# Optimization experiments

Measured on AMD Instinct MI355X. Metric: run time of the kernel, lower is better.

## Reference

```python
import jax, jax.numpy as jnp
import numpy as np

B, T, V, C, L, H = 4, 1024, 32000, 768, 6, 12
HD = C // H  # head size 64
EPS = 1e-5


def _ln(x, s, b):
    mu = jnp.mean(x, axis=-1, keepdims=True)
    var = jnp.var(x, axis=-1, keepdims=True)
    return (x - mu) * jax.lax.rsqrt(var + EPS) * s + b


def setup_inputs() -> dict:
    key = jax.random.key(0)
    ks = jax.random.split(key, 12)
    p = lambda k, shape: jax.random.normal(k, shape, jnp.float32) * 0.02
    return {
        "idx": jax.random.randint(ks[0], (B, T), 0, V),
        "targets": jax.random.randint(ks[1], (B, T), 0, V),
        "tok_emb": p(ks[2], (V, C)),
        "pos_emb": p(ks[3], (T, C)),
        "Wq": p(ks[4], (L, H, C, HD)),
        "Wk": p(ks[5], (L, H, C, HD)),
        "Wv": p(ks[6], (L, H, C, HD)),
        "ln1_s": jnp.ones((L, C), jnp.float32),
        "ln1_b": jnp.zeros((L, C), jnp.float32),
        "ln2_s": jnp.ones((L, C), jnp.float32),
        "ln2_b": jnp.zeros((L, C), jnp.float32),
        "W1": p(ks[7], (L, C, 4 * C)),
        "b1": jnp.zeros((L, 4 * C), jnp.float32),
        "W2": p(ks[8], (L, 4 * C, C)),
        "b2": jnp.zeros((L, C), jnp.float32),
        "lnf_s": jnp.ones((C,), jnp.float32),
        "lnf_b": jnp.zeros((C,), jnp.float32),
        "Wout": p(ks[9], (C, V)),
        "bout": jnp.zeros((V,), jnp.float32),
    }


def reference(idx, targets, tok_emb, pos_emb, Wq, Wk, Wv, ln1_s, ln1_b, ln2_s, ln2_b,
              W1, b1, W2, b2, lnf_s, lnf_b, Wout, bout):
    x = tok_emb[idx] + pos_emb[None, :T, :]  # [B,T,C]
    mask = jnp.tril(jnp.ones((T, T), bool))
    scale = HD ** -0.5
    for l in range(L):  # fixed small layer count
        xn = _ln(x, ln1_s[l], ln1_b[l])
        q = jnp.einsum('btc,hcd->bhtd', xn, Wq[l])
        k = jnp.einsum('btc,hcd->bhtd', xn, Wk[l])
        v = jnp.einsum('btc,hcd->bhtd', xn, Wv[l])
        scores = jnp.einsum('bhtd,bhsd->bhts', q, k) * scale
        scores = jnp.where(mask[None, None], scores, -jnp.inf)
        w = jax.nn.softmax(scores, axis=-1)
        att = jnp.einsum('bhts,bhsd->bhtd', w, v)
        # concat heads in order, matching torch.cat over ModuleList
        x = x + att.transpose(0, 2, 1, 3).reshape(B, T, C)
        xn2 = _ln(x, ln2_s[l], ln2_b[l])
        h = jax.nn.relu(jnp.einsum('btc,cf->btf', xn2, W1[l]) + b1[l])
        x = x + jnp.einsum('btf,fc->btc', h, W2[l]) + b2[l]
    x = _ln(x, lnf_s, lnf_b)
    logits = jnp.einsum('btc,cv->btv', x, Wout) + bout
    logits = logits.reshape(B * T, V)
    lp = jax.nn.log_softmax(logits, axis=-1)
    loss = -jnp.mean(lp[jnp.arange(B * T), targets.reshape(-1)])
    return logits, loss
```

## Files before the change

kernel.cpp:

```cpp
#include <hip/hip_runtime.h>
#include <hip/hip_bf16.h>


typedef __attribute__((ext_vector_type(8))) short          bh8;
typedef __attribute__((ext_vector_type(4))) unsigned short us4;
typedef __attribute__((ext_vector_type(4))) float          fl4;

__device__ inline unsigned short f2b(float f) {
  unsigned u = __float_as_uint(f);
  return (unsigned short)((u + 0x7fffu + ((u >> 16) & 1u)) >> 16);
}

__global__ __launch_bounds__(256) void embed_kernel(
    const int* __restrict__ idx, const float* __restrict__ tok,
    const float* __restrict__ pos, float* __restrict__ x)
{
  int i = blockIdx.x * 256 + threadIdx.x;
  int bt = i / 768, c = i - bt * 768;
  int t = bt & 1023;
  x[i] = tok[(size_t)idx[bt] * 768 + c] + pos[t * 768 + c];
}

__global__ __launch_bounds__(256) void ln_bf16_kernel(
    const float* __restrict__ x, const float* __restrict__ s,
    const float* __restrict__ b, unsigned short* __restrict__ out)
{
  __shared__ float red[256];
  int row = blockIdx.x, tid = threadIdx.x;
  const float* xr = x + (size_t)row * 768;
  float v0 = xr[tid], v1 = xr[tid + 256], v2 = xr[tid + 512];
  red[tid] = v0 + v1 + v2;
  __syncthreads();
  for (int o = 128; o > 0; o >>= 1) { if (tid < o) red[tid] += red[tid + o]; __syncthreads(); }
  float mu = red[0] * (1.0f / 768.0f);
  __syncthreads();
  float d0 = v0 - mu, d1 = v1 - mu, d2 = v2 - mu;
  red[tid] = d0 * d0 + d1 * d1 + d2 * d2;
  __syncthreads();
  for (int o = 128; o > 0; o >>= 1) { if (tid < o) red[tid] += red[tid + o]; __syncthreads(); }
  float inv = rsqrtf(red[0] * (1.0f / 768.0f) + 1e-5f);
  unsigned short* outr = out + (size_t)row * 768;
  outr[tid]       = f2b(d0 * inv * s[tid]       + b[tid]);
  outr[tid + 256] = f2b(d1 * inv * s[tid + 256] + b[tid + 256]);
  outr[tid + 512] = f2b(d2 * inv * s[tid + 512] + b[tid + 512]);
}

__global__ __launch_bounds__(256) void tconv_kernel(
    const float* __restrict__ src, unsigned short* __restrict__ dst,
    int K, int N)
{
  __shared__ float tt[64][65];
  int n0 = blockIdx.x * 64, k0 = blockIdx.y * 64;
  const float* s = src + (size_t)blockIdx.z * K * N;
  unsigned short* d = dst + (size_t)blockIdx.z * K * N;
  int tx = threadIdx.x & 63, g = threadIdx.x >> 6;
#pragma unroll
  for (int i = 0; i < 16; ++i) {
    int k = g * 16 + i;
    tt[k][tx] = s[(size_t)(k0 + k) * N + n0 + tx];
  }
  __syncthreads();
#pragma unroll
  for (int i = 0; i < 16; ++i) {
    int n = g * 16 + i;
    d[(size_t)(n0 + n) * K + k0 + tx] = f2b(tt[tx][n]);
  }
}

__global__ __launch_bounds__(256) void tqkv_kernel(
    const float* __restrict__ src, unsigned short* __restrict__ dst, int which)
{
  __shared__ float tt[64][65];
  int k0 = blockIdx.x * 64;
  int z = blockIdx.y;
  int l = z / 12, h = z - l * 12;
  const float* s = src + (size_t)z * 768 * 64;
  unsigned short* d = dst + (size_t)l * 2304 * 768 +
                      (size_t)(which * 768 + h * 64) * 768;
  int tx = threadIdx.x & 63, g = threadIdx.x >> 6;
#pragma unroll
  for (int i = 0; i < 16; ++i) {
    int k = g * 16 + i;
    tt[k][tx] = s[(size_t)(k0 + k) * 64 + tx];
  }
  __syncthreads();
#pragma unroll
  for (int i = 0; i < 16; ++i) {
    int n = g * 16 + i;
    d[(size_t)n * 768 + k0 + tx] = f2b(tt[tx][n]);
  }
}

template<int MODE>
__global__ __launch_bounds__(256) void gemm_bf16(
    const unsigned short* __restrict__ A, const unsigned short* __restrict__ Bt,
    const float* __restrict__ bias, float* __restrict__ OutF,
    unsigned short* __restrict__ OutH, int N, int K)
{
  __shared__ __align__(16) char As[128 * 64 * 2];
  __shared__ __align__(16) char Bs[128 * 64 * 2];
  const int tid = threadIdx.x;
  const int lane = tid & 63;
  const int wr = (tid >> 7) & 1, wc = (tid >> 6) & 1;
  const int m0 = blockIdx.y * 128, n0 = blockIdx.x * 128;
  const size_t Kb = (size_t)K * 2;

  fl4 acc[4][4] = {};
  const int o0 = tid * 16;
  const int rA = wr * 64 + (lane & 15);
  const int rB = wc * 64 + (lane & 15);
  const int kcol = (lane >> 4) << 4;
  const int sw = (lane & 7) << 4;

  auto ldAB = [&](int t, bh8* a, bh8* b) {
#pragma unroll
    for (int p = 0; p < 4; ++p) {
      int o = o0 + p * 4096;
      int row = o >> 7, col = o & 127;
      a[p] = *(const bh8*)((const char*)A + (size_t)(m0 + row) * Kb + (size_t)t * 128 + col);
      b[p] = *(const bh8*)((const char*)Bt + (size_t)(n0 + row) * Kb + (size_t)t * 128 + col);
    }
  };

  const int nK = K >> 6;
  bh8 ca[4], cb[4];
  ldAB(0, ca, cb);
  for (int t = 0; t < nK; ++t) {
    __syncthreads();
#pragma unroll
    for (int p = 0; p < 4; ++p) {
      int o = o0 + p * 4096;
      int row = o >> 7;
      int phys = o ^ ((row & 7) << 4);
      *(bh8*)(As + phys) = ca[p];
      *(bh8*)(Bs + phys) = cb[p];
    }
    __syncthreads();
    bh8 na[4], nb[4];
    const bool more = (t + 1 < nK);
    if (more) ldAB(t + 1, na, nb);
#pragma unroll
    for (int kh = 0; kh < 2; ++kh) {
      bh8 af[4], bf[4];
#pragma unroll
      for (int i = 0; i < 4; ++i) {
        af[i] = *(const bh8*)(As + (rA + i * 16) * 128 + ((kh * 64 + kcol) ^ sw));
        bf[i] = *(const bh8*)(Bs + (rB + i * 16) * 128 + ((kh * 64 + kcol) ^ sw));
      }
#pragma unroll
      for (int mi = 0; mi < 4; ++mi)
#pragma unroll
        for (int ni = 0; ni < 4; ++ni)
          acc[mi][ni] = __builtin_amdgcn_mfma_f32_16x16x32_bf16(
              af[mi], bf[ni], acc[mi][ni], 0, 0, 0);
    }
    if (more) {
#pragma unroll
      for (int p = 0; p < 4; ++p) { ca[p] = na[p]; cb[p] = nb[p]; }
    }
  }

  const int er = (lane >> 4) << 2;
  const int ec = lane & 15;
#pragma unroll
  for (int mi = 0; mi < 4; ++mi)
#pragma unroll
    for (int ni = 0; ni < 4; ++ni)
#pragma unroll
      for (int r = 0; r < 4; ++r) {
        int m = m0 + wr * 64 + mi * 16 + er + r;
        int n = n0 + wc * 64 + ni * 16 + ec;
        float v = acc[mi][ni][r];
        if (MODE == 0) {
          int which = n / 768, rem = n - which * 768;
          int hh = rem >> 6, dd = rem & 63;
          int bb = m >> 10, tt = m & 1023;
          size_t base = (size_t)(which * 48 + bb * 12 + hh) << 16;
          if (which == 2)
            OutH[base + (size_t)dd * 1024 + tt] = f2b(v);
          else
            OutH[base + (tt << 6) + dd] = f2b(v);
        } else if (MODE == 1) {
          v += bias[n]; v = fmaxf(v, 0.0f);
          OutH[(size_t)m * N + n] = f2b(v);
        } else {
          v += bias[n];
          OutF[(size_t)m * N + n] += v;
        }
      }
}

__global__ __launch_bounds__(256) void gemm_logits_bt(
    const unsigned short* __restrict__ A, const unsigned short* __restrict__ Bt,
    const float* __restrict__ bias, float* __restrict__ Out,
    float* __restrict__ pm, float* __restrict__ ps)
{
  __shared__ __align__(16) char As[256 * 64 * 2];
  __shared__ __align__(16) char Bs[64 * 64 * 2];
  const int tid = threadIdx.x, lane = tid & 63, wid = tid >> 6;
  const int n0 = blockIdx.x * 64;
  const size_t Kb = 1536;
  const int o0 = tid * 16;
  const int rA = wid * 64 + (lane & 15);
  const int rB = (lane & 15);
  const int kcol = (lane >> 4) << 4;
  const int sw = (lane & 7) << 4;
  const int ec = lane & 15, er = (lane >> 4) << 2;

  for (int mt = 0; mt < 8; ++mt) {
    const int m0 = blockIdx.y * 2048 + mt * 256;
    fl4 acc[4][4] = {};
    for (int t = 0; t < 12; ++t) {
      bh8 ra[8], rb[2];
#pragma unroll
      for (int p = 0; p < 8; ++p) {
        int o = o0 + p * 4096;
        int row = o >> 7, col = o & 127;
        ra[p] = *(const bh8*)((const char*)A + (size_t)(m0 + row) * Kb + (size_t)t * 128 + col);
      }
#pragma unroll
      for (int p = 0; p < 2; ++p) {
        int o = o0 + p * 4096;
        int row = o >> 7, col = o & 127;
        rb[p] = *(const bh8*)((const char*)Bt + (size_t)(n0 + row) * Kb + (size_t)t * 128 + col);
      }
      __syncthreads();
#pragma unroll
      for (int p = 0; p < 8; ++p) {
        int o = o0 + p * 4096;
        int row = o >> 7;
        *(bh8*)(As + (o ^ ((row & 7) << 4))) = ra[p];
      }
#pragma unroll
      for (int p = 0; p < 2; ++p) {
        int o = o0 + p * 4096;
        int row = o >> 7;
        *(bh8*)(Bs + (o ^ ((row & 7) << 4))) = rb[p];
      }
      __syncthreads();
#pragma unroll
      for (int kh = 0; kh < 2; ++kh) {
        bh8 af[4], bf[4];
#pragma unroll
        for (int i = 0; i < 4; ++i) {
          af[i] = *(const bh8*)(As + (rA + i * 16) * 128 + ((kh * 64 + kcol) ^ sw));
          bf[i] = *(const bh8*)(Bs + (rB + i * 16) * 128 + ((kh * 64 + kcol) ^ sw));
        }
#pragma unroll
        for (int mi = 0; mi < 4; ++mi)
#pragma unroll
          for (int ni = 0; ni < 4; ++ni)
            acc[mi][ni] = __builtin_amdgcn_mfma_f32_16x16x32_bf16(
                af[mi], bf[ni], acc[mi][ni], 0, 0, 0);
      }
    }
#pragma unroll
    for (int mi = 0; mi < 4; ++mi)
#pragma unroll
      for (int r = 0; r < 4; ++r) {
        int m = m0 + wid * 64 + mi * 16 + er + r;
        float tv[4];
#pragma unroll
        for (int ni = 0; ni < 4; ++ni) {
          int n = n0 + ni * 16 + ec;
          tv[ni] = acc[mi][ni][r] + bias[n];
          Out[(size_t)m * 32000 + n] = tv[ni];
        }
        if (pm) {
          float mx = fmaxf(fmaxf(tv[0], tv[1]), fmaxf(tv[2], tv[3]));
#pragma unroll
          for (int msk = 1; msk < 16; msk <<= 1)
            mx = fmaxf(mx, __shfl_xor(mx, msk));
          float ss = __expf(tv[0] - mx) + __expf(tv[1] - mx) +
                     __expf(tv[2] - mx) + __expf(tv[3] - mx);
#pragma unroll
          for (int msk = 1; msk < 16; msk <<= 1)
            ss += __shfl_xor(ss, msk);
          if (ec == 0) {
            pm[(size_t)m * 500 + blockIdx.x] = mx;
            ps[(size_t)m * 500 + blockIdx.x] = ss;
          }
        }
      }
  }
}

__global__ __launch_bounds__(256) void gemm_logits(
    const unsigned short* __restrict__ A, const float* __restrict__ W,
    const float* __restrict__ bias, float* __restrict__ Out)
{
  __shared__ __align__(16) char As[256 * 64 * 2];
  __shared__ __align__(16) char Bs[64 * 64 * 2];
  const int tid = threadIdx.x, lane = tid & 63, wid = tid >> 6;
  const int m0 = blockIdx.y * 256, n0 = blockIdx.x * 64;
  const size_t Kb = 1536;

  fl4 acc[4][4] = {};
  const int o0 = tid * 16;
  const int rA = wid * 64 + (lane & 15);
  const int rB = (lane & 15);
  const int kcol = (lane >> 4) << 4;
  const int sw = (lane & 7) << 4;
  const int bn = tid & 63, bg = tid >> 6;

  for (int t = 0; t < 12; ++t) {
    bh8 ra[8];
#pragma unroll
    for (int p = 0; p < 8; ++p) {
      int o = o0 + p * 4096;
      int row = o >> 7, col = o & 127;
      ra[p] = *(const bh8*)((const char*)A + (size_t)(m0 + row) * Kb + (size_t)t * 128 + col);
    }
    unsigned short rb[16];
#pragma unroll
    for (int p = 0; p < 4; ++p) {
      int q = p * 4 + bg;
#pragma unroll
      for (int i = 0; i < 4; ++i)
        rb[p * 4 + i] = f2b(W[(size_t)(t * 64 + q * 4 + i) * 32000 + n0 + bn]);
    }
    __syncthreads();
#pragma unroll
    for (int p = 0; p < 8; ++p) {
      int o = o0 + p * 4096;
      int row = o >> 7;
      *(bh8*)(As + (o ^ ((row & 7) << 4))) = ra[p];
    }
#pragma unroll
    for (int p = 0; p < 4; ++p) {
      int q = p * 4 + bg;
      int o = bn * 128 + q * 8;
      us4 w4 = { rb[p * 4], rb[p * 4 + 1], rb[p * 4 + 2], rb[p * 4 + 3] };
      *(us4*)(Bs + (o ^ ((bn & 7) << 4))) = w4;
    }
    __syncthreads();
#pragma unroll
    for (int kh = 0; kh < 2; ++kh) {
      bh8 af[4], bf[4];
#pragma unroll
      for (int i = 0; i < 4; ++i) {
        af[i] = *(const bh8*)(As + (rA + i * 16) * 128 + ((kh * 64 + kcol) ^ sw));
        bf[i] = *(const bh8*)(Bs + (rB + i * 16) * 128 + ((kh * 64 + kcol) ^ sw));
      }
#pragma unroll
      for (int mi = 0; mi < 4; ++mi)
#pragma unroll
        for (int ni = 0; ni < 4; ++ni)
          acc[mi][ni] = __builtin_amdgcn_mfma_f32_16x16x32_bf16(
              af[mi], bf[ni], acc[mi][ni], 0, 0, 0);
    }
    __syncthreads();
  }

  const int er = (lane >> 4) << 2, ec = lane & 15;
#pragma unroll
  for (int mi = 0; mi < 4; ++mi)
#pragma unroll
    for (int ni = 0; ni < 4; ++ni)
#pragma unroll
      for (int r = 0; r < 4; ++r) {
        int m = m0 + wid * 64 + mi * 16 + er + r;
        int n = n0 + ni * 16 + ec;
        Out[(size_t)m * 32000 + n] = acc[mi][ni][r] + bias[n];
      }
}

__global__ __launch_bounds__(128) void attn_mfma_kernel(
    const unsigned short* __restrict__ qkvb, float* __restrict__ x)
{
  __shared__ __align__(16) unsigned short Pls[2][32 * 72];
  __shared__ float MlLl[64];
  const int tid = threadIdx.x;
  const int lane = tid & 63, wv = tid >> 6;
  const int bh = blockIdx.y;
  const int b = bh / 12, h = bh - b * 12;
  const int qt = blockIdx.x, q0 = qt * 32;
  const int l15 = lane & 15, l4 = lane >> 4;
  const unsigned short* Qb = qkvb + ((size_t)bh << 16);
  const unsigned short* Kb = qkvb + ((size_t)(48 + bh) << 16);
  const unsigned short* Vb = qkvb + ((size_t)(96 + bh) << 16);
  unsigned short* Pl = Pls[wv];

  bh8 qf[2][2];
#pragma unroll
  for (int mi = 0; mi < 2; ++mi)
#pragma unroll
    for (int kh = 0; kh < 2; ++kh)
      qf[mi][kh] = *(const bh8*)(Qb + (size_t)(q0 + mi * 16 + l15) * 64 + kh * 32 + l4 * 8);

  fl4 o_acc[2][4] = {};
  fl4 m_run[2], l_run[2];
#pragma unroll
  for (int mi = 0; mi < 2; ++mi) {
    m_run[mi] = fl4{-3e38f, -3e38f, -3e38f, -3e38f};
    l_run[mi] = fl4{0.f, 0.f, 0.f, 0.f};
  }

  const int nkv = (qt >> 1) + 1;
  for (int j = wv; j < nkv; j += 2) {
    const int kv0 = j * 64;
    fl4 s[2][4] = {};
#pragma unroll
    for (int kh = 0; kh < 2; ++kh) {
      bh8 kf[4];
#pragma unroll
      for (int ni = 0; ni < 4; ++ni)
        kf[ni] = *(const bh8*)(Kb + (size_t)(kv0 + ni * 16 + l15) * 64 + kh * 32 + l4 * 8);
#pragma unroll
      for (int mi = 0; mi < 2; ++mi)
#pragma unroll
        for (int ni = 0; ni < 4; ++ni)
          s[mi][ni] = __builtin_amdgcn_mfma_f32_16x16x32_bf16(
              qf[mi][kh], kf[ni], s[mi][ni], 0, 0, 0);
    }

    const bool needmask = (kv0 + 63 > q0);
#pragma unroll
    for (int mi = 0; mi < 2; ++mi) {
#pragma unroll
      for (int r = 0; r < 4; ++r) {
        float mx = -3e38f;
#pragma unroll
        for (int ni = 0; ni < 4; ++ni) {
          float sv = s[mi][ni][r] * 0.125f;
          if (needmask) {
            int qg = q0 + mi * 16 + l4 * 4 + r;
            int kg = kv0 + ni * 16 + l15;
            if (kg > qg) sv = -3e38f;
          }
          s[mi][ni][r] = sv;
          mx = fmaxf(mx, sv);
        }
#pragma unroll
        for (int msk = 1; msk < 16; msk <<= 1)
          mx = fmaxf(mx, __shfl_xor(mx, msk));
        float mo = m_run[mi][r];
        float mn = fmaxf(mo, mx);
        float scale = __expf(mo - mn);
        float rsum = 0.f;
#pragma unroll
        for (int ni = 0; ni < 4; ++ni) {
          float p = __expf(s[mi][ni][r] - mn);
          s[mi][ni][r] = p;
          rsum += p;
        }
#pragma unroll
        for (int msk = 1; msk < 16; msk <<= 1)
          rsum += __shfl_xor(rsum, msk);
        m_run[mi][r] = mn;
        l_run[mi][r] = l_run[mi][r] * scale + rsum;
#pragma unroll
        for (int ni = 0; ni < 4; ++ni)
          o_acc[mi][ni][r] *= scale;
      }
#pragma unroll
      for (int ni = 0; ni < 4; ++ni)
#pragma unroll
        for (int r = 0; r < 4; ++r)
          Pl[(mi * 16 + l4 * 4 + r) * 72 + ni * 16 + l15] = f2b(s[mi][ni][r]);
    }

#pragma unroll
    for (int kh = 0; kh < 2; ++kh) {
      bh8 pf[2], vf[4];
#pragma unroll
      for (int mi = 0; mi < 2; ++mi)
        pf[mi] = *(const bh8*)(Pl + (mi * 16 + l15) * 72 + kh * 32 + l4 * 8);
#pragma unroll
      for (int ni = 0; ni < 4; ++ni)
        vf[ni] = *(const bh8*)(Vb + (size_t)(ni * 16 + l15) * 1024 + kv0 + kh * 32 + l4 * 8);
#pragma unroll
      for (int mi = 0; mi < 2; ++mi)
#pragma unroll
        for (int ni = 0; ni < 4; ++ni)
          o_acc[mi][ni] = __builtin_amdgcn_mfma_f32_16x16x32_bf16(
              pf[mi], vf[ni], o_acc[mi][ni], 0, 0, 0);
    }
  }

  __syncthreads();
  float* Ol = (float*)&Pls[0][0];
  if (wv == 1) {
#pragma unroll
    for (int mi = 0; mi < 2; ++mi)
#pragma unroll
      for (int r = 0; r < 4; ++r) {
        int row = mi * 16 + l4 * 4 + r;
        if (l15 == 0) { MlLl[row] = m_run[mi][r]; MlLl[32 + row] = l_run[mi][r]; }
#pragma unroll
        for (int ni = 0; ni < 4; ++ni)
          Ol[row * 68 + ni * 16 + l15] = o_acc[mi][ni][r];
      }
  }
  __syncthreads();
  if (wv == 0) {
#pragma unroll
    for (int mi = 0; mi < 2; ++mi)
#pragma unroll
      for (int r = 0; r < 4; ++r) {
        int row = mi * 16 + l4 * 4 + r;
        float m1 = MlLl[row], l1 = MlLl[32 + row];
        float m0v = m_run[mi][r];
        float mn = fmaxf(m0v, m1);
        float s0 = __expf(m0v - mn), s1 = __expf(m1 - mn);
        float inv = 1.0f / (l_run[mi][r] * s0 + l1 * s1);
        int q = q0 + row;
#pragma unroll
        for (int ni = 0; ni < 4; ++ni) {
          int d = ni * 16 + l15;
          float o = o_acc[mi][ni][r] * s0 + Ol[row * 68 + ni * 16 + l15] * s1;
          x[(size_t)(b * 1024 + q) * 768 + h * 64 + d] += o * inv;
        }
      }
  }
}

__global__ __launch_bounds__(256) void lossmerge_kernel(
    const float* __restrict__ pm, const float* __restrict__ ps,
    const float* __restrict__ logits, const int* __restrict__ targets,
    float* __restrict__ lrow)
{
  __shared__ float red[256];
  int row = blockIdx.x, tid = threadIdx.x;
  const float* pmr = pm + (size_t)row * 500;
  const float* psr = ps + (size_t)row * 500;
  float m = -3e38f;
  for (int i = tid; i < 500; i += 256) m = fmaxf(m, pmr[i]);
  red[tid] = m; __syncthreads();
  for (int o = 128; o > 0; o >>= 1) { if (tid < o) red[tid] = fmaxf(red[tid], red[tid + o]); __syncthreads(); }
  m = red[0]; __syncthreads();
  float s = 0.f;
  for (int i = tid; i < 500; i += 256) s += psr[i] * __expf(pmr[i] - m);
  red[tid] = s; __syncthreads();
  for (int o = 128; o > 0; o >>= 1) { if (tid < o) red[tid] += red[tid + o]; __syncthreads(); }
  if (tid == 0) {
    float lse = m + logf(red[0]);
    lrow[row] = (lse - logits[(size_t)row * 32000 + targets[row]]) * (1.0f / 4096.0f);
  }
}

__global__ __launch_bounds__(256) void lossrow_kernel(
    const float* __restrict__ logits, const int* __restrict__ targets,
    float* __restrict__ lrow)
{
  __shared__ float red[256];
  int row = blockIdx.x, tid = threadIdx.x;
  const float* lr = logits + (size_t)row * 32000;
  const float4* lr4 = (const float4*)lr;
  float lmax = -1e30f;
  for (int i = tid; i < 8000; i += 256) {
    float4 v = lr4[i];
    lmax = fmaxf(fmaxf(lmax, fmaxf(v.x, v.y)), fmaxf(v.z, v.w));
  }
  red[tid] = lmax; __syncthreads();
  for (int o = 128; o > 0; o >>= 1) { if (tid < o) red[tid] = fmaxf(red[tid], red[tid + o]); __syncthreads(); }
  float m = red[0]; __syncthreads();
  float ls = 0.f;
  for (int i = tid; i < 8000; i += 256) {
    float4 v = lr4[i];
    ls += expf(v.x - m) + expf(v.y - m) + expf(v.z - m) + expf(v.w - m);
  }
  red[tid] = ls; __syncthreads();
  for (int o = 128; o > 0; o >>= 1) { if (tid < o) red[tid] += red[tid + o]; __syncthreads(); }
  if (tid == 0) {
    float lse = m + logf(red[0]);
    lrow[row] = (lse - lr[targets[row]]) * (1.0f / 4096.0f);
  }
}

__global__ __launch_bounds__(256) void lossred_kernel(
    const float* __restrict__ lrow, float* __restrict__ out)
{
  __shared__ float red[256];
  int tid = threadIdx.x;
  float s = 0.f;
  for (int i = tid; i < 4096; i += 256) s += lrow[i];
  red[tid] = s; __syncthreads();
  for (int o = 128; o > 0; o >>= 1) { if (tid < o) red[tid] += red[tid + o]; __syncthreads(); }
  if (tid == 0) out[0] = red[0];
}

extern "C" void kernel_launch(void* const* d_in, const int* in_sizes, int n_in,
                              void* d_out, int out_size, void* d_ws, size_t ws_size,
                              hipStream_t stream)
{
  (void)in_sizes; (void)n_in; (void)out_size;
  const int Bq = 4, T = 1024, V = 32000, C = 768, L = 6;
  const int M = Bq * T;

  const int*   idx     = (const int*)d_in[0];
  const int*   targets = (const int*)d_in[1];
  const float* tok     = (const float*)d_in[2];
  const float* pos     = (const float*)d_in[3];
  const float* Wq      = (const float*)d_in[4];
  const float* Wk      = (const float*)d_in[5];
  const float* Wv      = (const float*)d_in[6];
  const float* ln1s    = (const float*)d_in[7];
  const float* ln1b    = (const float*)d_in[8];
  const float* ln2s    = (const float*)d_in[9];
  const float* ln2b    = (const float*)d_in[10];
  const float* W1      = (const float*)d_in[11];
  const float* b1      = (const float*)d_in[12];
  const float* W2      = (const float*)d_in[13];
  const float* b2      = (const float*)d_in[14];
  const float* lnfs    = (const float*)d_in[15];
  const float* lnfb    = (const float*)d_in[16];
  const float* Wout    = (const float*)d_in[17];
  const float* bout    = (const float*)d_in[18];
  float* out = (float*)d_out;

  char* ob = (char*)d_out;
  size_t oo = 0;
  auto oa = [&](size_t bytes) {
    void* p = ob + oo; oo += (bytes + 255) & ~(size_t)255; return p;
  };
  float*          x     = (float*)oa((size_t)M * C * 4);
  unsigned short* qkvb  = (unsigned short*)oa((size_t)3 * 48 * 65536 * 2);
  unsigned short* hb    = (unsigned short*)oa((size_t)M * 3072 * 2);
  unsigned short* Wqkvt = (unsigned short*)oa((size_t)L * 2304 * C * 2);
  unsigned short* W1t   = (unsigned short*)oa((size_t)L * C * 3072 * 2);
  unsigned short* W2t   = (unsigned short*)oa((size_t)L * C * 3072 * 2);

  char* wp = (char*)d_ws;
  unsigned short* xnb  = (unsigned short*)wp;
  float*          lrow = (float*)(wp + (size_t)M * C * 2);
  float*          pm   = (float*)(wp + (size_t)M * C * 2 + 16384);
  float*          ps   = pm + (size_t)M * 500;
  const size_t off_wbt_full  = (size_t)M * C * 2 + 16384 + (size_t)M * 500 * 8;
  const size_t off_wbt_small = (size_t)M * C * 2 + 16384;
  const size_t wbt_bytes = (size_t)V * C * 2;
  const bool full_ws = ws_size >= off_wbt_full + wbt_bytes;
  const bool wbt_ok  = full_ws || ws_size >= off_wbt_small + wbt_bytes;
  unsigned short* Wbt = (unsigned short*)(wp + (full_ws ? off_wbt_full
                                                        : off_wbt_small));

  embed_kernel<<<(M * C) / 256, 256, 0, stream>>>(idx, tok, pos, x);
  tqkv_kernel<<<dim3(12, 72), 256, 0, stream>>>(Wq, Wqkvt, 0);
  tqkv_kernel<<<dim3(12, 72), 256, 0, stream>>>(Wk, Wqkvt, 1);
  tqkv_kernel<<<dim3(12, 72), 256, 0, stream>>>(Wv, Wqkvt, 2);
  tconv_kernel<<<dim3(48, 12, 6), 256, 0, stream>>>(W1, W1t, C, 3072);
  tconv_kernel<<<dim3(12, 48, 6), 256, 0, stream>>>(W2, W2t, 3072, C);
  if (wbt_ok)
    tconv_kernel<<<dim3(500, 12, 1), 256, 0, stream>>>(Wout, Wbt, C, V);

  for (int l = 0; l < L; ++l) {
    ln_bf16_kernel<<<M, 256, 0, stream>>>(x, ln1s + l * C, ln1b + l * C, xnb);
    gemm_bf16<0><<<dim3(18, 32), 256, 0, stream>>>(
        xnb, Wqkvt + (size_t)l * 2304 * C, nullptr, nullptr, qkvb, 2304, C);
    attn_mfma_kernel<<<dim3(32, 48), 128, 0, stream>>>(qkvb, x);
    ln_bf16_kernel<<<M, 256, 0, stream>>>(x, ln2s + l * C, ln2b + l * C, xnb);
    gemm_bf16<1><<<dim3(24, 32), 256, 0, stream>>>(
        xnb, W1t + (size_t)l * C * 3072, b1 + (size_t)l * 3072, nullptr, hb, 3072, C);
    gemm_bf16<2><<<dim3(6, 32), 256, 0, stream>>>(
        hb, W2t + (size_t)l * C * 3072, b2 + (size_t)l * C, x, nullptr, C, 3072);
  }

  ln_bf16_kernel<<<M, 256, 0, stream>>>(x, lnfs, lnfb, xnb);
  if (wbt_ok)
    gemm_logits_bt<<<dim3(500, 2), 256, 0, stream>>>(
        xnb, Wbt, bout, out, full_ws ? pm : nullptr, full_ws ? ps : nullptr);
  else
    gemm_logits<<<dim3(500, 16), 256, 0, stream>>>(xnb, Wout, bout, out);

  if (full_ws && wbt_ok)
    lossmerge_kernel<<<M, 256, 0, stream>>>(pm, ps, out, targets, lrow);
  else
    lossrow_kernel<<<M, 256, 0, stream>>>(out, targets, lrow);
  lossred_kernel<<<1, 256, 0, stream>>>(lrow, out + (size_t)M * V);
}
```

Before: 1.684 ms.

## Retile logits GEMM to 128x128 blocks with register-prefetched K tiles

The logits GEMM moves from 64-column blocks that each looped over eight 256-row M tiles (grid 500x2) to square 128x128 tiles with a 2x2 wave layout over a much larger grid (250x32). Each K step's global loads for the next tile are now issued into registers before the current tile's MFMAs, so load latency overlaps with compute. The partial max/sum outputs keep their 64-column granularity by indexing with blockIdx.x*2+wc. The larger grid should fill the device better and balance A/B reuse, but the per-block M loop that reused B tiles across eight M tiles is gone, and register pressure goes up.

```diff
diff --git a/kernel.cpp b/kernel.cpp
--- a/kernel.cpp
+++ b/kernel.cpp
@@ -195,94 +195,99 @@
     const float* __restrict__ bias, float* __restrict__ Out,
     float* __restrict__ pm, float* __restrict__ ps)
 {
-  __shared__ __align__(16) char As[256 * 64 * 2];
-  __shared__ __align__(16) char Bs[64 * 64 * 2];
-  const int tid = threadIdx.x, lane = tid & 63, wid = tid >> 6;
-  const int n0 = blockIdx.x * 64;
+  __shared__ __align__(16) char As[128 * 64 * 2];
+  __shared__ __align__(16) char Bs[128 * 64 * 2];
+  const int tid = threadIdx.x;
+  const int lane = tid & 63;
+  const int wr = (tid >> 7) & 1, wc = (tid >> 6) & 1;
+  const int m0 = blockIdx.y * 128, n0 = blockIdx.x * 128;
   const size_t Kb = 1536;
+
+  fl4 acc[4][4] = {};
   const int o0 = tid * 16;
-  const int rA = wid * 64 + (lane & 15);
-  const int rB = (lane & 15);
+  const int rA = wr * 64 + (lane & 15);
+  const int rB = wc * 64 + (lane & 15);
   const int kcol = (lane >> 4) << 4;
   const int sw = (lane & 7) << 4;
-  const int ec = lane & 15, er = (lane >> 4) << 2;
-
-  for (int mt = 0; mt < 8; ++mt) {
-    const int m0 = blockIdx.y * 2048 + mt * 256;
-    fl4 acc[4][4] = {};
-    for (int t = 0; t < 12; ++t) {
-      bh8 ra[8], rb[2];
-#pragma unroll
-      for (int p = 0; p < 8; ++p) {
-        int o = o0 + p * 4096;
-        int row = o >> 7, col = o & 127;
-        ra[p] = *(const bh8*)((const char*)A + (size_t)(m0 + row) * Kb + (size_t)t * 128 + col);
-      }
-#pragma unroll
-      for (int p = 0; p < 2; ++p) {
-        int o = o0 + p * 4096;
-        int row = o >> 7, col = o & 127;
-        rb[p] = *(const bh8*)((const char*)Bt + (size_t)(n0 + row) * Kb + (size_t)t * 128 + col);
-      }
-      __syncthreads();
-#pragma unroll
-      for (int p = 0; p < 8; ++p) {
-        int o = o0 + p * 4096;
-        int row = o >> 7;
-        *(bh8*)(As + (o ^ ((row & 7) << 4))) = ra[p];
-      }
-#pragma unroll
-      for (int p = 0; p < 2; ++p) {
-        int o = o0 + p * 4096;
-        int row = o >> 7;
-        *(bh8*)(Bs + (o ^ ((row & 7) << 4))) = rb[p];
-      }
-      __syncthreads();
-#pragma unroll
-      for (int kh = 0; kh < 2; ++kh) {
-        bh8 af[4], bf[4];
-#pragma unroll
-        for (int i = 0; i < 4; ++i) {
-          af[i] = *(const bh8*)(As + (rA + i * 16) * 128 + ((kh * 64 + kcol) ^ sw));
-          bf[i] = *(const bh8*)(Bs + (rB + i * 16) * 128 + ((kh * 64 + kcol) ^ sw));
+
+  auto ldAB = [&](int t, bh8* a, bh8* b) {
+#pragma unroll
+    for (int p = 0; p < 4; ++p) {
+      int o = o0 + p * 4096;
+      int row = o >> 7, col = o & 127;
+      a[p] = *(const bh8*)((const char*)A + (size_t)(m0 + row) * Kb + (size_t)t * 128 + col);
+      b[p] = *(const bh8*)((const char*)Bt + (size_t)(n0 + row) * Kb + (size_t)t * 128 + col);
+    }
+  };
+
+  const int nK = 12;
+  bh8 ca[4], cb[4];
+  ldAB(0, ca, cb);
+  for (int t = 0; t < nK; ++t) {
+    __syncthreads();
+#pragma unroll
+    for (int p = 0; p < 4; ++p) {
+      int o = o0 + p * 4096;
+      int row = o >> 7;
+      int phys = o ^ ((row & 7) << 4);
+      *(bh8*)(As + phys) = ca[p];
+      *(bh8*)(Bs + phys) = cb[p];
+    }
+    __syncthreads();
+    bh8 na[4], nb[4];
+    const bool more = (t + 1 < nK);
+    if (more) ldAB(t + 1, na, nb);
+#pragma unroll
+    for (int kh = 0; kh < 2; ++kh) {
+      bh8 af[4], bf[4];
+#pragma unroll
+      for (int i = 0; i < 4; ++i) {
+        af[i] = *(const bh8*)(As + (rA + i * 16) * 128 + ((kh * 64 + kcol) ^ sw));
+        bf[i] = *(const bh8*)(Bs + (rB + i * 16) * 128 + ((kh * 64 + kcol) ^ sw));
+      }
+#pragma unroll
+      for (int mi = 0; mi < 4; ++mi)
+#pragma unroll
+        for (int ni = 0; ni < 4; ++ni)
+          acc[mi][ni] = __builtin_amdgcn_mfma_f32_16x16x32_bf16(
+              af[mi], bf[ni], acc[mi][ni], 0, 0, 0);
+    }
+    if (more) {
+#pragma unroll
+      for (int p = 0; p < 4; ++p) { ca[p] = na[p]; cb[p] = nb[p]; }
+    }
+  }
+
+  const int er = (lane >> 4) << 2;
+  const int ec = lane & 15;
+#pragma unroll
+  for (int mi = 0; mi < 4; ++mi)
+#pragma unroll
+    for (int r = 0; r < 4; ++r) {
+      int m = m0 + wr * 64 + mi * 16 + er + r;
+      float tv[4];
+#pragma unroll
+      for (int ni = 0; ni < 4; ++ni) {
+        int n = n0 + wc * 64 + ni * 16 + ec;
+        tv[ni] = acc[mi][ni][r] + bias[n];
+        Out[(size_t)m * 32000 + n] = tv[ni];
+      }
+      if (pm) {
+        float mx = fmaxf(fmaxf(tv[0], tv[1]), fmaxf(tv[2], tv[3]));
+#pragma unroll
+        for (int msk = 1; msk < 16; msk <<= 1)
+          mx = fmaxf(mx, __shfl_xor(mx, msk));
+        float ss = __expf(tv[0] - mx) + __expf(tv[1] - mx) +
+                   __expf(tv[2] - mx) + __expf(tv[3] - mx);
+#pragma unroll
+        for (int msk = 1; msk < 16; msk <<= 1)
+          ss += __shfl_xor(ss, msk);
+        if (ec == 0) {
+          pm[(size_t)m * 500 + blockIdx.x * 2 + wc] = mx;
+          ps[(size_t)m * 500 + blockIdx.x * 2 + wc] = ss;
         }
-#pragma unroll
-        for (int mi = 0; mi < 4; ++mi)
-#pragma unroll
-          for (int ni = 0; ni < 4; ++ni)
-            acc[mi][ni] = __builtin_amdgcn_mfma_f32_16x16x32_bf16(
-                af[mi], bf[ni], acc[mi][ni], 0, 0, 0);
-      }
-    }
-#pragma unroll
-    for (int mi = 0; mi < 4; ++mi)
-#pragma unroll
-      for (int r = 0; r < 4; ++r) {
-        int m = m0 + wid * 64 + mi * 16 + er + r;
-        float tv[4];
-#pragma unroll
-        for (int ni = 0; ni < 4; ++ni) {
-          int n = n0 + ni * 16 + ec;
-          tv[ni] = acc[mi][ni][r] + bias[n];
-          Out[(size_t)m * 32000 + n] = tv[ni];
-        }
-        if (pm) {
-          float mx = fmaxf(fmaxf(tv[0], tv[1]), fmaxf(tv[2], tv[3]));
-#pragma unroll
-          for (int msk = 1; msk < 16; msk <<= 1)
-            mx = fmaxf(mx, __shfl_xor(mx, msk));
-          float ss = __expf(tv[0] - mx) + __expf(tv[1] - mx) +
-                     __expf(tv[2] - mx) + __expf(tv[3] - mx);
-#pragma unroll
-          for (int msk = 1; msk < 16; msk <<= 1)
-            ss += __shfl_xor(ss, msk);
-          if (ec == 0) {
-            pm[(size_t)m * 500 + blockIdx.x] = mx;
-            ps[(size_t)m * 500 + blockIdx.x] = ss;
-          }
-        }
-      }
-  }
+      }
+    }
 }
 
 __global__ __launch_bounds__(256) void gemm_logits(
@@ -657,7 +662,7 @@
 
   ln_bf16_kernel<<<M, 256, 0, stream>>>(x, lnfs, lnfb, xnb);
   if (wbt_ok)
-    gemm_logits_bt<<<dim3(500, 2), 256, 0, stream>>>(
+    gemm_logits_bt<<<dim3(250, 32), 256, 0, stream>>>(
         xnb, Wbt, bout, out, full_ws ? pm : nullptr, full_ws ? ps : nullptr);
   else
     gemm_logits<<<dim3(500, 16), 256, 0, stream>>>(xnb, Wout, bout, out);
```

Result: no change. 1.675 ms (-0.5%).
